# Performance work log

Hardware: AMD Instinct MI355X
Metric: run time of the kernel (lower is better)

## Reference

```python
import jax, jax.numpy as jnp
import numpy as np

B, C, H, W = 1024, 3, 224, 220
ROWS, COLS = 4, 5          # _factorize_patches(20)
P = ROWS * COLS            # num_patches = 20
HID = 32                   # FeatureNet hidden


def setup_inputs() -> dict:
    key = jax.random.key(0)
    kx, k1, k2, k3, k4 = jax.random.split(key, 5)
    x = jax.random.normal(kx, (B, C, H, W), dtype=jnp.float32)
    # per-patch FeatureNet params: Linear(1,HID) -> ReLU -> Linear(HID,1)
    lim1 = 1.0  # kaiming-uniform bound for fan_in=1 is sqrt(1/1); exact init unimportant
    w1 = jax.random.uniform(k1, (P, HID), jnp.float32, -lim1, lim1)
    b1 = jax.random.uniform(k2, (P, HID), jnp.float32, -lim1, lim1)
    lim2 = 1.0 / np.sqrt(HID)
    w2 = jax.random.uniform(k3, (P, HID), jnp.float32, -lim2, lim2)
    b2 = jax.random.uniform(k4, (P,), jnp.float32, -lim2, lim2)
    return {"x": x, "w1": w1, "b1": b1, "w2": w2, "b2": b2}


def reference(x, w1, b1, w2, b2):
    Bc = x.shape[0]
    ph, pw = H // ROWS, W // COLS
    # vectorized patch mean-pool over (C, ph, pw): [B, rows, cols] -> [B, P]
    xp = x.reshape(Bc, C, ROWS, ph, COLS, pw)
    feats = xp.mean(axis=(1, 3, 5)).reshape(Bc, P)  # [B, P]
    # per-patch scalar MLP: relu(f*w1 + b1) @ w2 + b2, batched over P
    h = jax.nn.relu(feats[:, :, None] * w1[None] + b1[None])  # [B, P, HID]
    contribs = jnp.einsum('bph,ph->bp', h, w2) + b2[None]      # [B, P]
    score = contribs.sum(axis=1, keepdims=True)                # [B, 1]
    return score, contribs
```

## Files before the change

kernel.cpp:

```cpp
#include <hip/hip_runtime.h>

#define CCH 3
#define HH 224
#define WW 220
#define PH 56
#define PW 44
#define ROWS 4
#define COLS 5
#define NP 20
#define HID 32

#define W4   (WW / 4)
#define HW4  (HH * WW / 4)
#define PW4  (PW / 4)
#define N4   (CCH * PH * PW4)
#define PATCH_ELEMS 7392.0f

__global__ __launch_bounds__(256) void patch_mlp_kernel(
    const float* __restrict__ x,
    const float* __restrict__ w1, const float* __restrict__ b1,
    const float* __restrict__ w2, const float* __restrict__ b2,
    float* __restrict__ out, int B)
{
    const int blk = blockIdx.x;
    const int b   = blk / NP;
    const int p   = blk - b * NP;
    const int pr  = p / COLS;
    const int pc  = p - pr * COLS;

    const float4* base4 = (const float4*)x
                        + (size_t)b * (size_t)(CCH * HH * WW / 4)
                        + pr * (PH * W4)
                        + pc * PW4;

    const int tid = threadIdx.x;

    float partial = 0.f;
    for (int t = tid; t < N4; t += 256) {
        int row = t / PW4;
        int col = t - row * PW4;
        int c   = row / PH;
        int r   = row - c * PH;
        float4 v = base4[c * HW4 + r * W4 + col];
        partial += v.x + v.y + v.z + v.w;
    }

    for (int off = 32; off; off >>= 1)
        partial += __shfl_down(partial, off, 64);

    __shared__ float swarp[4];
    __shared__ float sfeat;
    const int wid = tid >> 6;
    if ((tid & 63) == 0) swarp[wid] = partial;
    __syncthreads();
    if (tid == 0) {
        float tot = swarp[0] + swarp[1] + swarp[2] + swarp[3];
        sfeat = tot / PATCH_ELEMS;
    }
    __syncthreads();

    if (tid < 64) {
        const float f = sfeat;
        float term = 0.f;
        if (tid < HID) {
            float h = fmaf(f, w1[p * HID + tid], b1[p * HID + tid]);
            term = fmaxf(h, 0.f) * w2[p * HID + tid];
        }
        for (int off = 32; off; off >>= 1)
            term += __shfl_down(term, off, 64);
        if (tid == 0)
            out[B + (size_t)b * NP + p] = term + b2[p];
    }
}

__global__ __launch_bounds__(256) void score_kernel(
    const float* __restrict__ contribs, float* __restrict__ score, int B)
{
    int b = blockIdx.x * blockDim.x + threadIdx.x;
    if (b < B) {
        float s = 0.f;
        #pragma unroll
        for (int p = 0; p < NP; p++)
            s += contribs[(size_t)b * NP + p];
        score[b] = s;
    }
}

extern "C" void kernel_launch(void* const* d_in, const int* in_sizes, int n_in,
                              void* d_out, int out_size, void* d_ws, size_t ws_size,
                              hipStream_t stream)
{
    const float* x  = (const float*)d_in[0];
    const float* w1 = (const float*)d_in[1];
    const float* b1 = (const float*)d_in[2];
    const float* w2 = (const float*)d_in[3];
    const float* b2 = (const float*)d_in[4];
    float* out = (float*)d_out;

    const int B = in_sizes[0] / (CCH * HH * WW);

    patch_mlp_kernel<<<B * NP, 256, 0, stream>>>(x, w1, b1, w2, b2, out, B);
    score_kernel<<<(B + 255) / 256, 256, 0, stream>>>(out + B, out, B);
}
```

Measured before the change: 773.7 us.

## Fuse patch pooling, MLP and score into one block-per-image kernel

Replaces the one-block-per-patch kernel plus separate score kernel with a single kernel where each block handles a whole image. Lanes read full contiguous image rows as float4, accumulate per patch-row partials, reduce through shared memory into the 20 patch means, then run the per-patch MLP and score sum in the same block. This aims to improve coalescing and remove the second launch. The trade-off is fewer blocks (one per image) and 9 idle lanes per wave, which may limit memory-level parallelism.

Result: no change. 762.8 us (-1.4%).

```diff
diff --git a/kernel.cpp b/kernel.cpp
--- a/kernel.cpp
+++ b/kernel.cpp
@@ -3,86 +3,83 @@
 #define CCH 3
 #define HH 224
 #define WW 220
-#define PH 56
-#define PW 44
 #define ROWS 4
 #define COLS 5
 #define NP 20
 #define HID 32
+#define PH 56
+#define PW 44
 
-#define W4   (WW / 4)
-#define HW4  (HH * WW / 4)
-#define PW4  (PW / 4)
-#define N4   (CCH * PH * PW4)
-#define PATCH_ELEMS 7392.0f
+#define W4      (WW / 4)
+#define IMG4    (CCH * HH * W4)
+#define INV_N   (1.0f / 7392.0f)
 
-__global__ __launch_bounds__(256) void patch_mlp_kernel(
+__global__ __launch_bounds__(256) void fused_patch_nam_kernel(
     const float* __restrict__ x,
     const float* __restrict__ w1, const float* __restrict__ b1,
     const float* __restrict__ w2, const float* __restrict__ b2,
     float* __restrict__ out, int B)
 {
-    const int blk = blockIdx.x;
-    const int b   = blk / NP;
-    const int p   = blk - b * NP;
-    const int pr  = p / COLS;
-    const int pc  = p - pr * COLS;
+    const int b    = blockIdx.x;
+    const int tid  = threadIdx.x;
+    const int wid  = tid >> 6;
+    const int lane = tid & 63;
 
-    const float4* base4 = (const float4*)x
-                        + (size_t)b * (size_t)(CCH * HH * WW / 4)
-                        + pr * (PH * W4)
-                        + pc * PW4;
+    const float4* img4 = (const float4*)x + (size_t)b * IMG4;
 
-    const int tid = threadIdx.x;
+    float part[ROWS] = {0.f, 0.f, 0.f, 0.f};
 
-    float partial = 0.f;
-    for (int t = tid; t < N4; t += 256) {
-        int row = t / PW4;
-        int col = t - row * PW4;
-        int c   = row / PH;
-        int r   = row - c * PH;
-        float4 v = base4[c * HW4 + r * W4 + col];
-        partial += v.x + v.y + v.z + v.w;
+    if (lane < W4) {
+        for (int c = 0; c < CCH; ++c) {
+            const float4* pbase = img4 + (size_t)(c * HH + wid) * W4 + lane;
+            for (int j = 0; j < PH / 4; ++j) {
+                const float4* rb = pbase + (j * 4) * W4;
+                #pragma unroll
+                for (int pr = 0; pr < ROWS; ++pr) {
+                    float4 v = rb[pr * PH * W4];
+                    part[pr] += (v.x + v.y) + (v.z + v.w);
+                }
+            }
+        }
     }
 
-    for (int off = 32; off; off >>= 1)
-        partial += __shfl_down(partial, off, 64);
-
-    __shared__ float swarp[4];
-    __shared__ float sfeat;
-    const int wid = tid >> 6;
-    if ((tid & 63) == 0) swarp[wid] = partial;
-    __syncthreads();
-    if (tid == 0) {
-        float tot = swarp[0] + swarp[1] + swarp[2] + swarp[3];
-        sfeat = tot / PATCH_ELEMS;
+    __shared__ float red[4][ROWS][W4 + 1];
+    if (lane < W4) {
+        #pragma unroll
+        for (int pr = 0; pr < ROWS; ++pr)
+            red[wid][pr][lane] = part[pr];
     }
     __syncthreads();
 
-    if (tid < 64) {
-        const float f = sfeat;
-        float term = 0.f;
-        if (tid < HID) {
-            float h = fmaf(f, w1[p * HID + tid], b1[p * HID + tid]);
-            term = fmaxf(h, 0.f) * w2[p * HID + tid];
-        }
-        for (int off = 32; off; off >>= 1)
-            term += __shfl_down(term, off, 64);
-        if (tid == 0)
-            out[B + (size_t)b * NP + p] = term + b2[p];
-    }
-}
-
-__global__ __launch_bounds__(256) void score_kernel(
-    const float* __restrict__ contribs, float* __restrict__ score, int B)
-{
-    int b = blockIdx.x * blockDim.x + threadIdx.x;
-    if (b < B) {
+    __shared__ float contribs_s[NP];
+    if (tid < NP) {
+        const int pr = tid / COLS;
+        const int pc = tid - pr * COLS;
         float s = 0.f;
         #pragma unroll
-        for (int p = 0; p < NP; p++)
-            s += contribs[(size_t)b * NP + p];
-        score[b] = s;
+        for (int w = 0; w < 4; ++w)
+            #pragma unroll
+            for (int l = 0; l < W4 / COLS; ++l)
+                s += red[w][pr][pc * (W4 / COLS) + l];
+        const float f = s * INV_N;
+
+        float acc = 0.f;
+        #pragma unroll
+        for (int k = 0; k < HID; ++k) {
+            float h = fmaf(f, w1[tid * HID + k], b1[tid * HID + k]);
+            acc = fmaf(fmaxf(h, 0.f), w2[tid * HID + k], acc);
+        }
+        const float contrib = acc + b2[tid];
+        out[B + (size_t)b * NP + tid] = contrib;
+        contribs_s[tid] = contrib;
+    }
+    __syncthreads();
+
+    if (tid == 0) {
+        float s = 0.f;
+        #pragma unroll
+        for (int p = 0; p < NP; ++p) s += contribs_s[p];
+        out[b] = s;
     }
 }
 
@@ -99,6 +96,5 @@
 
     const int B = in_sizes[0] / (CCH * HH * WW);
 
-    patch_mlp_kernel<<<B * NP, 256, 0, stream>>>(x, w1, b1, w2, b2, out, B);
-    score_kernel<<<(B + 255) / 256, 256, 0, stream>>>(out + B, out, B);
+    fused_patch_nam_kernel<<<B, 256, 0, stream>>>(x, w1, b1, w2, b2, out, B);
 }
```
